# Optimization experiments

Hardware: AMD Instinct MI355X
Metric: run time of the kernel (lower is better)

Reference implementation:

```python
import jax, jax.numpy as jnp
import numpy as np

N, K, B, D, T = 30000, 32, 8, 256, 10
NC = T + 1            # int_small_classes
LB_COL, UB_COL = 21, 22
INF = 1e18


def _ln(x, g, b, eps=1e-5):
    m = jnp.mean(x, axis=-1, keepdims=True)
    v = jnp.mean((x - m) ** 2, axis=-1, keepdims=True)
    return (x - m) * jax.lax.rsqrt(v + eps) * g + b


def _head(x, ng, nb, W1, b1, W2, b2, Wh, bh):
    # LayerNorm -> Linear -> GELU -> Linear -> GELU -> residual -> head (dropout off: eval)
    h = _ln(x, ng, nb)
    h = jax.nn.gelu(h @ W1.T + b1, approximate=False)
    h = jax.nn.gelu(h @ W2.T + b2, approximate=False)
    return (x + h) @ Wh.T + bh


def setup_inputs():
    key = jax.random.key(0)
    ks = jax.random.split(key, 32)
    s = 0.05
    inp = {}
    inp['evolved_tokens'] = jax.random.normal(ks[0], (B * K, D), jnp.float32)
    inp['var_batch'] = jnp.sort(jax.random.randint(ks[1], (N,), 0, B))
    aw = jax.random.uniform(ks[2], (N, K), jnp.float32)
    inp['attn_weights'] = aw / aw.sum(-1, keepdims=True)
    inp['var_types'] = jax.random.randint(ks[3], (N,), 0, 3)
    inp['z_var_0'] = jax.random.normal(ks[4], (N, D), jnp.float32)
    vf = 0.1 * jax.random.normal(ks[5], (N, 23), jnp.float32)
    lb = jnp.floor(jax.random.uniform(ks[6], (N,), minval=-5.0, maxval=0.0))
    ub = lb + jnp.floor(jax.random.uniform(ks[7], (N,), minval=0.0, maxval=30.0))
    ub = jnp.where(jax.random.uniform(ks[8], (N,)) < 0.1, 1e19, ub)
    inp['variable_features'] = vf.at[:, LB_COL].set(lb).at[:, UB_COL].set(ub)
    # deslice proj + fusion norm
    inp['Wp'] = s * jax.random.normal(ks[9], (D, D), jnp.float32)
    inp['bp'] = jnp.zeros((D,), jnp.float32)
    inp['fn_g'] = jnp.ones((D,), jnp.float32)
    inp['fn_b'] = jnp.zeros((D,), jnp.float32)
    # three decoder heads
    i = 10
    for name, out in (('bin', 1), ('ints', NC), ('intl', 1)):
        inp[name + '_ng'] = jnp.ones((D,), jnp.float32)
        inp[name + '_nb'] = jnp.zeros((D,), jnp.float32)
        inp[name + '_W1'] = s * jax.random.normal(ks[i], (D, D), jnp.float32)
        inp[name + '_b1'] = jnp.zeros((D,), jnp.float32)
        inp[name + '_W2'] = s * jax.random.normal(ks[i + 1], (D, D), jnp.float32)
        inp[name + '_b2'] = jnp.zeros((D,), jnp.float32)
        inp[name + '_Wh'] = s * jax.random.normal(ks[i + 2], (out, D), jnp.float32)
        inp[name + '_bh'] = (jnp.full((out,), -0.5, jnp.float32) if name == 'bin'
                             else jnp.zeros((out,), jnp.float32))
        i += 3
    return inp


def reference(evolved_tokens, var_batch, attn_weights, var_types, z_var_0,
              variable_features, Wp, bp, fn_g, fn_b,
              bin_ng, bin_nb, bin_W1, bin_b1, bin_W2, bin_b2, bin_Wh, bin_bh,
              ints_ng, ints_nb, ints_W1, ints_b1, ints_W2, ints_b2, ints_Wh, ints_bh,
              intl_ng, intl_nb, intl_W1, intl_b1, intl_W2, intl_b2, intl_Wh, intl_bh):
    # 1. deslice: attn_weights @ projected evolved tokens of the variable's graph
    proj = evolved_tokens @ Wp.T + bp          # [B*K, D]
    tok3 = proj.reshape(B, K, D)
    z_des = jnp.einsum('nk,nkd->nd', attn_weights, tok3[var_batch])  # [N, D]
    # 2. residual fusion + LayerNorm
    z_out = _ln(z_des + z_var_0, fn_g, fn_b)
    # 3. routing (extract_int_routing)
    lb = variable_features[:, LB_COL]
    ub = variable_features[:, UB_COL]
    is_int = var_types == 2
    finite = (jnp.abs(lb) < INF) & (jnp.abs(ub) < INF)
    mask_int_small = is_int & finite & ((ub - lb) <= T)
    mask_int_large = is_int & ~mask_int_small
    mask_bin = var_types == 1
    offsets = jnp.floor(lb)                                   # [N]
    ranges = jnp.clip(jnp.ceil(ub) - offsets + 1.0, 1.0, NC).astype(jnp.int32)  # [N]
    # 4. decode. Heads are evaluated densely on all N rows; the original's
    #    gather->MLP->scatter equals row-selection of these dense outputs.
    prob_bin = jax.nn.sigmoid(_head(z_out, bin_ng, bin_nb, bin_W1, bin_b1,
                                    bin_W2, bin_b2, bin_Wh, bin_bh))   # [N, 1]
    logits = _head(z_out, ints_ng, ints_nb, ints_W1, ints_b1,
                   ints_W2, ints_b2, ints_Wh, ints_bh)                 # [N, NC]
    valid = jnp.arange(NC)[None, :] < ranges[:, None]
    logits = jnp.where(valid, logits, -1e9)  # dynamic logit masking of invalid classes
    pred_large = _head(z_out, intl_ng, intl_nb, intl_W1, intl_b1,
                       intl_W2, intl_b2, intl_Wh, intl_bh)             # [N, 1]
    return (z_out, prob_bin, logits, pred_large,
            mask_bin, mask_int_small, mask_int_large, offsets, ranges)
```

## Files before the change

kernel.cpp:

```cpp
#include <hip/hip_runtime.h>
#include <math.h>

#define NV   30000
#define DD   256
#define KK   32
#define NCLS 11
#define NT   469

#define OZ  0
#define OPB 7680000
#define OLG 7710000
#define OPL 8040000
#define OMB 8070000
#define OMS 8100000
#define OML 8130000
#define OOF 8160000
#define ORG 8190000

typedef __bf16 bf16x8 __attribute__((ext_vector_type(8)));
typedef float  f32x4  __attribute__((ext_vector_type(4)));

__device__ __forceinline__ unsigned short f2b(float f) {
    unsigned u = __float_as_uint(f);
    u += 0x7fffu + ((u >> 16) & 1u);
    return (unsigned short)(u >> 16);
}

__device__ __forceinline__ float gelu_f(float x) {
    float x2 = x * x;
    float m = x * __builtin_fmaf(-0.0713548163f, x2, -1.5957691216f);
    float e = __expf(m);
    return x * __builtin_amdgcn_rcpf(1.0f + e);
}

__device__ __forceinline__ int swz(int row) { return (row + (row >> 3)) & 7; }
__device__ __forceinline__ int lidx(int row, int col) {
    return row * 256 + ((((col) >> 3) ^ swz(row)) << 3) + (col & 7);
}

struct WP {
    const float *W1, *ng, *nb, *b1, *W2, *Wh;
    unsigned short *W1e, *W2b, *Whb;
    float *b1e, *swh;
    int nc;
};

__global__ void k_prep(const float* __restrict__ et, const float* __restrict__ Wp,
                       const float* __restrict__ bp, unsigned short* __restrict__ projb,
                       const float* __restrict__ vf, const int* __restrict__ vt,
                       float* __restrict__ out,
                       WP wa, WP wb, WP wc) {
    __shared__ float es[DD];
    __shared__ float red[4], red2[4];
    if (blockIdx.y == 0) {
        int r = blockIdx.x, c = threadIdx.x;
        es[c] = et[r * DD + c];
        __syncthreads();
        const float4* w4 = (const float4*)(Wp + c * DD);
        float acc = bp[c];
#pragma unroll 16
        for (int d = 0; d < DD / 4; ++d) {
            float4 w = w4[d];
            acc += es[4 * d] * w.x + es[4 * d + 1] * w.y + es[4 * d + 2] * w.z + es[4 * d + 3] * w.w;
        }
        projb[r * DD + c] = f2b(acc);
        return;
    }
    if (blockIdx.y == 4) {
        int n = blockIdx.x * 256 + threadIdx.x;
        if (n < NV) {
            float lb = vf[n * 23 + 21], ub = vf[n * 23 + 22];
            int t = vt[n];
            bool is_int = (t == 2);
            bool finite = (fabsf(lb) < 1e18f) && (fabsf(ub) < 1e18f);
            bool small_ = is_int && finite && (ub - lb <= 10.0f);
            float off = floorf(lb);
            float rngf = ceilf(ub) - off + 1.0f;
            rngf = fminf(fmaxf(rngf, 1.0f), (float)NCLS);
            out[OMB + n] = (t == 1) ? 1.0f : 0.0f;
            out[OMS + n] = small_ ? 1.0f : 0.0f;
            out[OML + n] = (is_int && !small_) ? 1.0f : 0.0f;
            out[OOF + n] = off;
            out[ORG + n] = (float)((int)rngf);
        }
        return;
    }
    WP wp = (blockIdx.y == 1) ? wa : ((blockIdx.y == 2) ? wb : wc);
    int j = blockIdx.x, d = threadIdx.x;
    float v1 = wp.W1[j * DD + d];
    wp.W1e[j * DD + d] = f2b(v1 * wp.ng[d]);
    wp.W2b[j * DD + d] = f2b(wp.W2[j * DD + d]);
    float p2 = 0.f;
    if (j < 16) {
        p2 = (j < wp.nc) ? wp.Wh[j * DD + d] : 0.f;
        wp.Whb[j * DD + d] = f2b(p2);
    }
    float p = v1 * wp.nb[d];
#pragma unroll
    for (int m = 1; m < 64; m <<= 1) { p += __shfl_xor(p, m); p2 += __shfl_xor(p2, m); }
    if ((d & 63) == 0) { red[d >> 6] = p; red2[d >> 6] = p2; }
    __syncthreads();
    if (d == 0) {
        wp.b1e[j] = wp.b1[j] + red[0] + red[1] + red[2] + red[3];
        if (j < 16) wp.swh[j] = red2[0] + red2[1] + red2[2] + red2[3];
    }
}

__global__ __launch_bounds__(256)
void k_zout(const unsigned short* __restrict__ projb, const int* __restrict__ vb,
            const float* __restrict__ aw, const float* __restrict__ z0,
            const float* __restrict__ g, const float* __restrict__ b,
            float* __restrict__ out, unsigned short* __restrict__ zhat,
            float2* __restrict__ zstat) {
    int wv = threadIdx.x >> 6, lane = threadIdx.x & 63;
    int n0r = blockIdx.x * 8 + wv * 2;
    if (n0r >= NV) return;
    bool ok1 = (n0r + 1) < NV;
    int b0 = vb[n0r];
    int b1i = ok1 ? vb[n0r + 1] : b0;
    float aw0 = aw[(size_t)n0r * KK + (lane & 31)];
    float aw1 = ok1 ? aw[(size_t)(n0r + 1) * KK + (lane & 31)] : 0.f;
    const ushort4* pr0 = (const ushort4*)(projb + (size_t)b0 * KK * DD);
    const ushort4* pr1 = (const ushort4*)(projb + (size_t)b1i * KK * DD);
    float4 acc0 = ((const float4*)(z0 + (size_t)n0r * DD))[lane];
    float4 acc1 = ok1 ? ((const float4*)(z0 + (size_t)(n0r + 1) * DD))[lane]
                      : make_float4(0.f, 0.f, 0.f, 0.f);
#pragma unroll 4
    for (int k = 0; k < KK; ++k) {
        float a0 = __shfl(aw0, k), a1 = __shfl(aw1, k);
        ushort4 p0 = pr0[k * 64 + lane];
        ushort4 p1 = pr1[k * 64 + lane];
        acc0.x += a0 * __uint_as_float((unsigned)p0.x << 16);
        acc0.y += a0 * __uint_as_float((unsigned)p0.y << 16);
        acc0.z += a0 * __uint_as_float((unsigned)p0.z << 16);
        acc0.w += a0 * __uint_as_float((unsigned)p0.w << 16);
        acc1.x += a1 * __uint_as_float((unsigned)p1.x << 16);
        acc1.y += a1 * __uint_as_float((unsigned)p1.y << 16);
        acc1.z += a1 * __uint_as_float((unsigned)p1.z << 16);
        acc1.w += a1 * __uint_as_float((unsigned)p1.w << 16);
    }
    float s0 = acc0.x + acc0.y + acc0.z + acc0.w;
    float q0 = acc0.x * acc0.x + acc0.y * acc0.y + acc0.z * acc0.z + acc0.w * acc0.w;
    float s1 = acc1.x + acc1.y + acc1.z + acc1.w;
    float q1 = acc1.x * acc1.x + acc1.y * acc1.y + acc1.z * acc1.z + acc1.w * acc1.w;
#pragma unroll
    for (int m = 1; m < 64; m <<= 1) {
        s0 += __shfl_xor(s0, m); q0 += __shfl_xor(q0, m);
        s1 += __shfl_xor(s1, m); q1 += __shfl_xor(q1, m);
    }
    float4 g4 = ((const float4*)g)[lane], b4 = ((const float4*)b)[lane];
#pragma unroll
    for (int rr = 0; rr < 2; ++rr) {
        int n = n0r + rr;
        if (rr && !ok1) break;
        float4 acc = rr ? acc1 : acc0;
        float s = rr ? s1 : s0, q = rr ? q1 : q0;
        float mean = s * (1.f / DD);
        float var  = q * (1.f / DD) - mean * mean;
        float rs   = rsqrtf(var + 1e-5f);
        float4 z;
        z.x = (acc.x - mean) * rs * g4.x + b4.x;
        z.y = (acc.y - mean) * rs * g4.y + b4.y;
        z.z = (acc.z - mean) * rs * g4.z + b4.z;
        z.w = (acc.w - mean) * rs * g4.w + b4.w;
        ((float4*)(out + OZ + (size_t)n * DD))[lane] = z;
        float s2 = z.x + z.y + z.z + z.w;
        float q2 = z.x * z.x + z.y * z.y + z.z * z.z + z.w * z.w;
#pragma unroll
        for (int m = 1; m < 64; m <<= 1) { s2 += __shfl_xor(s2, m); q2 += __shfl_xor(q2, m); }
        float m2 = s2 * (1.f / DD);
        float v2 = q2 * (1.f / DD) - m2 * m2;
        float r2 = rsqrtf(v2 + 1e-5f);
        ushort4 zh;
        zh.x = f2b((z.x - m2) * r2); zh.y = f2b((z.y - m2) * r2);
        zh.z = f2b((z.z - m2) * r2); zh.w = f2b((z.w - m2) * r2);
        int rl = n & 63;
        int c = lane >> 1;
        int pc = (c & ~7) | ((c & 7) ^ swz(rl));
        *(ushort4*)(zhat + (size_t)(n & ~63) * 256 + rl * 256 + pc * 8 + (lane & 1) * 4) = zh;
        if (lane == 0) zstat[n] = make_float2((v2 + 1e-5f) * r2, m2);
    }
}

struct HeadP {
    const unsigned short *W1e, *W2b, *Whb;
    const float *b1e, *b2, *bh, *swh;
    int nc;
};

__global__ __launch_bounds__(512, 4)
void k_heads(const unsigned short* __restrict__ zhat, const float2* __restrict__ zstat,
             const float* __restrict__ ranges,
             HeadP h0, HeadP h1p, HeadP h2p,
             float* __restrict__ opb, float* __restrict__ olg, float* __restrict__ opl) {
    __shared__ unsigned short hl[64 * 256];
    __shared__ float b1s[DD], b2s[DD];
    __shared__ float rs2s[64], m2s[64];
    __shared__ float swhs[16], bhs[16];

    int head = blockIdx.x / NT;
    int tile = blockIdx.x % NT;
    HeadP hp = (head == 0) ? h0 : ((head == 1) ? h1p : h2p);
    int nc = hp.nc;
    int n0 = tile * 64;
    int tid = threadIdx.x;

    {
        const uint4* src = (const uint4*)(zhat + (size_t)n0 * 256);
        uint4* dst = (uint4*)hl;
#pragma unroll
        for (int j = 0; j < 4; ++j) dst[tid + j * 512] = src[tid + j * 512];
    }
    if (tid < 256) b1s[tid] = hp.b1e[tid];
    else           b2s[tid - 256] = hp.b2[tid - 256];
    if (tid < 64) {
        int n = n0 + tid;
        float2 st = (n < NV) ? zstat[n] : make_float2(0.f, 0.f);
        rs2s[tid] = st.x; m2s[tid] = st.y;
    } else if (tid < 80) {
        swhs[tid - 64] = hp.swh[tid - 64];
    } else if (tid < 96) {
        int o = tid - 80;
        bhs[o] = (o < nc) ? hp.bh[o] : 0.f;
    }

    int lane = tid & 63, wv = tid >> 6;
    int l15 = lane & 15, lq = lane >> 4;
    int nb0 = wv * 32;

    f32x4 acc[4][2];
#pragma unroll
    for (int mt = 0; mt < 4; ++mt)
#pragma unroll
        for (int nt = 0; nt < 2; ++nt) acc[mt][nt] = f32x4{0.f, 0.f, 0.f, 0.f};

    __syncthreads();

    {
        const unsigned short* Bb = hp.W1e + (size_t)(nb0 + l15) * DD + lq * 8;
        bf16x8 b[2][2], a[4];
#pragma unroll
        for (int nt = 0; nt < 2; ++nt) b[0][nt] = *(const bf16x8*)(Bb + nt * 16 * DD);
#pragma unroll
        for (int ks = 0; ks < 8; ++ks) {
            int cur = ks & 1;
            if (ks < 7) {
#pragma unroll
                for (int nt = 0; nt < 2; ++nt)
                    b[cur ^ 1][nt] = *(const bf16x8*)(Bb + nt * 16 * DD + (ks + 1) * 32);
            }
            int ck = ks * 4 + lq;
#pragma unroll
            for (int mt = 0; mt < 4; ++mt) {
                int row = mt * 16 + l15;
                int ph = (ck & ~7) | ((ck & 7) ^ swz(row));
                a[mt] = *(const bf16x8*)(hl + row * 256 + ph * 8);
            }
#pragma unroll
            for (int nt = 0; nt < 2; ++nt)
#pragma unroll
                for (int mt = 0; mt < 4; ++mt)
                    acc[mt][nt] = __builtin_amdgcn_mfma_f32_16x16x32_bf16(a[mt], b[cur][nt], acc[mt][nt], 0, 0, 0);
        }
    }
    __syncthreads();

#pragma unroll
    for (int nt = 0; nt < 2; ++nt) {
        int col = nb0 + nt * 16 + l15;
        float bias = b1s[col];
#pragma unroll
        for (int mt = 0; mt < 4; ++mt)
#pragma unroll
            for (int r = 0; r < 4; ++r) {
                int row = mt * 16 + lq * 4 + r;
                hl[lidx(row, col)] = f2b(gelu_f(acc[mt][nt][r] + bias));
            }
    }
    __syncthreads();

#pragma unroll
    for (int mt = 0; mt < 4; ++mt)
#pragma unroll
        for (int nt = 0; nt < 2; ++nt) acc[mt][nt] = f32x4{0.f, 0.f, 0.f, 0.f};
    {
        const unsigned short* Bb = hp.W2b + (size_t)(nb0 + l15) * DD + lq * 8;
        bf16x8 b[2][2], a[4];
#pragma unroll
        for (int nt = 0; nt < 2; ++nt) b[0][nt] = *(const bf16x8*)(Bb + nt * 16 * DD);
#pragma unroll
        for (int ks = 0; ks < 8; ++ks) {
            int cur = ks & 1;
            if (ks < 7) {
#pragma unroll
                for (int nt = 0; nt < 2; ++nt)
                    b[cur ^ 1][nt] = *(const bf16x8*)(Bb + nt * 16 * DD + (ks + 1) * 32);
            }
            int ck = ks * 4 + lq;
#pragma unroll
            for (int mt = 0; mt < 4; ++mt) {
                int row = mt * 16 + l15;
                int ph = (ck & ~7) | ((ck & 7) ^ swz(row));
                a[mt] = *(const bf16x8*)(hl + row * 256 + ph * 8);
            }
#pragma unroll
            for (int nt = 0; nt < 2; ++nt)
#pragma unroll
                for (int mt = 0; mt < 4; ++mt)
                    acc[mt][nt] = __builtin_amdgcn_mfma_f32_16x16x32_bf16(a[mt], b[cur][nt], acc[mt][nt], 0, 0, 0);
        }
    }

#pragma unroll
    for (int nt = 0; nt < 2; ++nt) {
        float bias = b2s[nb0 + nt * 16 + l15];
#pragma unroll
        for (int mt = 0; mt < 4; ++mt)
#pragma unroll
            for (int r = 0; r < 4; ++r)
                acc[mt][nt][r] = gelu_f(acc[mt][nt][r] + bias);
    }
    __syncthreads();

#pragma unroll
    for (int nt = 0; nt < 2; ++nt) {
        int col = nb0 + nt * 16 + l15;
#pragma unroll
        for (int mt = 0; mt < 4; ++mt)
#pragma unroll
            for (int r = 0; r < 4; ++r) {
                int row = mt * 16 + lq * 4 + r;
                hl[lidx(row, col)] = f2b(acc[mt][nt][r]);
            }
    }

    f32x4 accP[4], accZ[4];
#pragma unroll
    for (int mt = 0; mt < 4; ++mt) { accP[mt] = f32x4{0.f, 0.f, 0.f, 0.f}; accZ[mt] = f32x4{0.f, 0.f, 0.f, 0.f}; }
    {
        const unsigned short* Wb = hp.Whb + (size_t)l15 * DD + nb0 + lq * 8;
        const unsigned short* zt = zhat + (size_t)n0 * 256;
        bf16x8 bP = *(const bf16x8*)(Wb);
        int ck = (nb0 >> 3) + lq;
#pragma unroll
        for (int mt = 0; mt < 4; ++mt) {
            int row = mt * 16 + l15;
            int ph = (ck & ~7) | ((ck & 7) ^ swz(row));
            bf16x8 aP = *(const bf16x8*)(hl + row * 256 + ph * 8);
            bf16x8 aZ = *(const bf16x8*)(zt + row * 256 + ph * 8);
            accP[mt] = __builtin_amdgcn_mfma_f32_16x16x32_bf16(aP, bP, accP[mt], 0, 0, 0);
            accZ[mt] = __builtin_amdgcn_mfma_f32_16x16x32_bf16(aZ, bP, accZ[mt], 0, 0, 0);
        }
    }
    __syncthreads();

#pragma unroll
    for (int mt = 0; mt < 4; ++mt) {
        int rb = mt * 16 + lq * 4;
#pragma unroll
        for (int r = 0; r < 4; ++r) {
            float pv = accP[mt][r] + rs2s[rb + r] * accZ[mt][r];
            float* pp = (float*)(hl + (rb + r) * 256 + nb0);
            pp[l15] = pv;
        }
    }
    __syncthreads();

    for (int idx = tid; idx < 64 * nc; idx += 512) {
        int row, o;
        if (nc == 1) { row = idx; o = 0; }
        else { row = idx / NCLS; o = idx - row * NCLS; }
        int n = n0 + row;
        if (n < NV) {
            float val = bhs[o] + m2s[row] * swhs[o];
#pragma unroll
            for (int w2 = 0; w2 < 8; ++w2)
                val += ((const float*)(hl + row * 256 + w2 * 32))[o];
            if (head == 0)      opb[n] = __builtin_amdgcn_rcpf(1.f + __expf(-val));
            else if (head == 2) opl[n] = val;
            else {
                int rng = (int)ranges[n];
                olg[n * NCLS + o] = (o < rng) ? val : -1e9f;
            }
        }
    }
}

extern "C" void kernel_launch(void* const* d_in, const int* in_sizes, int n_in,
                              void* d_out, int out_size, void* d_ws, size_t ws_size,
                              hipStream_t stream) {
    const float* et = (const float*)d_in[0];
    const int*   vb = (const int*)d_in[1];
    const float* aw = (const float*)d_in[2];
    const int*   vt = (const int*)d_in[3];
    const float* z0 = (const float*)d_in[4];
    const float* vf = (const float*)d_in[5];
    const float* Wp = (const float*)d_in[6];
    const float* bp = (const float*)d_in[7];
    const float* fg = (const float*)d_in[8];
    const float* fb = (const float*)d_in[9];
    float* out = (float*)d_out;

    char* ws = (char*)d_ws;
    unsigned short* projb = (unsigned short*)ws;
    float* b1e           = (float*)(ws + 131072);
    unsigned short* W1e  = (unsigned short*)(ws + 134144);
    unsigned short* W2b  = (unsigned short*)(ws + 527360);
    unsigned short* Whb  = (unsigned short*)(ws + 920576);
    float* swh           = (float*)(ws + 945152);
    float2* zstat        = (float2*)(ws + 945408);
    unsigned short* zhat = (unsigned short*)(ws + 1185536);

    WP wps[3];
    for (int h = 0; h < 3; ++h) {
        wps[h].W1 = (const float*)d_in[12 + 8 * h];
        wps[h].ng = (const float*)d_in[10 + 8 * h];
        wps[h].nb = (const float*)d_in[11 + 8 * h];
        wps[h].b1 = (const float*)d_in[13 + 8 * h];
        wps[h].W2 = (const float*)d_in[14 + 8 * h];
        wps[h].Wh = (const float*)d_in[16 + 8 * h];
        wps[h].W1e = W1e + h * 65536;
        wps[h].W2b = W2b + h * 65536;
        wps[h].Whb = Whb + h * 4096;
        wps[h].b1e = b1e + h * 256;
        wps[h].swh = swh + h * 16;
        wps[h].nc  = (h == 1) ? NCLS : 1;
    }
    k_prep<<<dim3(256, 5), 256, 0, stream>>>(et, Wp, bp, projb, vf, vt, out,
                                             wps[0], wps[1], wps[2]);

    k_zout<<<3750, 256, 0, stream>>>(projb, vb, aw, z0, fg, fb, out, zhat, zstat);

    HeadP hps[3];
    for (int h = 0; h < 3; ++h) {
        hps[h].W1e = W1e + h * 65536;
        hps[h].W2b = W2b + h * 65536;
        hps[h].Whb = Whb + h * 4096;
        hps[h].b1e = b1e + h * 256;
        hps[h].b2  = (const float*)d_in[15 + 8 * h];
        hps[h].bh  = (const float*)d_in[17 + 8 * h];
        hps[h].swh = swh + h * 16;
        hps[h].nc  = (h == 1) ? NCLS : 1;
    }
    k_heads<<<3 * NT, 512, 0, stream>>>(zhat, zstat, out + ORG,
                                        hps[0], hps[1], hps[2],
                                        out + OPB, out + OLG, out + OPL);
}
```

Measured before the change: 250.2 us.

## Compute z_out gather-sum as MFMA GEMM and precompute head residual projection

k_zout now builds a 64x256 bf16 attention matrix per tile (attention weights scattered to the batch's 32 columns) and multiplies it by a transposed projection with MFMA, replacing per-row scalar gathers of projected tokens. The same kernel also computes the residual term zhat·Wh for all three heads and stores it, so k_heads no longer re-reads zhat for that. k_heads swaps operand roles so weights are the A operand, uses two LDS buffers to cut a barrier, and reorganises the final reduction. The costs are a larger LDS footprint, a mostly-zero dense A matrix doing wasted MFMA work, and bf16 rounding of the attention weights.

```diff
diff --git a/kernel.cpp b/kernel.cpp
--- a/kernel.cpp
+++ b/kernel.cpp
@@ -37,6 +37,9 @@
 __device__ __forceinline__ int lidx(int row, int col) {
     return row * 256 + ((((col) >> 3) ^ swz(row)) << 3) + (col & 7);
 }
+__device__ __forceinline__ int physchunk(int ck, int row) {
+    return (ck & ~7) | ((ck & 7) ^ swz(row));
+}
 
 struct WP {
     const float *W1, *ng, *nb, *b1, *W2, *Wh;
@@ -46,7 +49,7 @@
 };
 
 __global__ void k_prep(const float* __restrict__ et, const float* __restrict__ Wp,
-                       const float* __restrict__ bp, unsigned short* __restrict__ projb,
+                       const float* __restrict__ bp, unsigned short* __restrict__ projT,
                        const float* __restrict__ vf, const int* __restrict__ vt,
                        float* __restrict__ out,
                        WP wa, WP wb, WP wc) {
@@ -63,7 +66,7 @@
             float4 w = w4[d];
             acc += es[4 * d] * w.x + es[4 * d + 1] * w.y + es[4 * d + 2] * w.z + es[4 * d + 3] * w.w;
         }
-        projb[r * DD + c] = f2b(acc);
+        projT[c * DD + r] = f2b(acc);
         return;
     }
     if (blockIdx.y == 4) {
@@ -106,281 +109,369 @@
     }
 }
 
-__global__ __launch_bounds__(256)
-void k_zout(const unsigned short* __restrict__ projb, const int* __restrict__ vb,
+__global__ __launch_bounds__(512)
+void k_zout(const unsigned short* __restrict__ projT, const int* __restrict__ vb,
             const float* __restrict__ aw, const float* __restrict__ z0,
             const float* __restrict__ g, const float* __restrict__ b,
+            const unsigned short* __restrict__ Whb, const float* __restrict__ swh,
             float* __restrict__ out, unsigned short* __restrict__ zhat,
-            float2* __restrict__ zstat) {
-    int wv = threadIdx.x >> 6, lane = threadIdx.x & 63;
-    int n0r = blockIdx.x * 8 + wv * 2;
-    if (n0r >= NV) return;
-    bool ok1 = (n0r + 1) < NV;
-    int b0 = vb[n0r];
-    int b1i = ok1 ? vb[n0r + 1] : b0;
-    float aw0 = aw[(size_t)n0r * KK + (lane & 31)];
-    float aw1 = ok1 ? aw[(size_t)(n0r + 1) * KK + (lane & 31)] : 0.f;
-    const ushort4* pr0 = (const ushort4*)(projb + (size_t)b0 * KK * DD);
-    const ushort4* pr1 = (const ushort4*)(projb + (size_t)b1i * KK * DD);
-    float4 acc0 = ((const float4*)(z0 + (size_t)n0r * DD))[lane];
-    float4 acc1 = ok1 ? ((const float4*)(z0 + (size_t)(n0r + 1) * DD))[lane]
-                      : make_float4(0.f, 0.f, 0.f, 0.f);
-#pragma unroll 4
-    for (int k = 0; k < KK; ++k) {
-        float a0 = __shfl(aw0, k), a1 = __shfl(aw1, k);
-        ushort4 p0 = pr0[k * 64 + lane];
-        ushort4 p1 = pr1[k * 64 + lane];
-        acc0.x += a0 * __uint_as_float((unsigned)p0.x << 16);
-        acc0.y += a0 * __uint_as_float((unsigned)p0.y << 16);
-        acc0.z += a0 * __uint_as_float((unsigned)p0.z << 16);
-        acc0.w += a0 * __uint_as_float((unsigned)p0.w << 16);
-        acc1.x += a1 * __uint_as_float((unsigned)p1.x << 16);
-        acc1.y += a1 * __uint_as_float((unsigned)p1.y << 16);
-        acc1.z += a1 * __uint_as_float((unsigned)p1.z << 16);
-        acc1.w += a1 * __uint_as_float((unsigned)p1.w << 16);
-    }
-    float s0 = acc0.x + acc0.y + acc0.z + acc0.w;
-    float q0 = acc0.x * acc0.x + acc0.y * acc0.y + acc0.z * acc0.z + acc0.w * acc0.w;
-    float s1 = acc1.x + acc1.y + acc1.z + acc1.w;
-    float q1 = acc1.x * acc1.x + acc1.y * acc1.y + acc1.z * acc1.z + acc1.w * acc1.w;
-#pragma unroll
-    for (int m = 1; m < 64; m <<= 1) {
-        s0 += __shfl_xor(s0, m); q0 += __shfl_xor(q0, m);
-        s1 += __shfl_xor(s1, m); q1 += __shfl_xor(q1, m);
-    }
-    float4 g4 = ((const float4*)g)[lane], b4 = ((const float4*)b)[lane];
-#pragma unroll
-    for (int rr = 0; rr < 2; ++rr) {
-        int n = n0r + rr;
-        if (rr && !ok1) break;
-        float4 acc = rr ? acc1 : acc0;
-        float s = rr ? s1 : s0, q = rr ? q1 : q0;
+            float* __restrict__ zwhT) {
+    __shared__ unsigned short Al[64 * 256];
+    __shared__ float sqs[64 * 8], sqq[64 * 8];
+    __shared__ float mvm[64], mvr[64], sig[64];
+    __shared__ float gs[DD], bs[DD];
+    __shared__ float swhs[48];
+    int tid = threadIdx.x;
+    int lane = tid & 63, wv = tid >> 6;
+    int l15 = lane & 15, lq = lane >> 4;
+    int n0 = blockIdx.x * 64;
+
+    if (tid < 256) gs[tid] = g[tid];
+    else           bs[tid - 256] = b[tid - 256];
+    if (tid < 48) swhs[tid] = swh[tid];
+    {
+        uint4 z4 = make_uint4(0, 0, 0, 0);
+        uint4* dst = (uint4*)Al;
+#pragma unroll
+        for (int j = 0; j < 4; ++j) dst[tid + j * 512] = z4;
+    }
+    __syncthreads();
+    {
+        int r = tid >> 3, sub = tid & 7;
+        int n = n0 + r;
+        if (n < NV) {
+            int bb = vb[n];
+            float4 a4 = *(const float4*)(aw + (size_t)n * KK + sub * 4);
+            int j0 = bb * 32 + sub * 4;
+            int phys = r * 256 + (physchunk(j0 >> 3, r) << 3) + (j0 & 7);
+            ushort4 u;
+            u.x = f2b(a4.x); u.y = f2b(a4.y); u.z = f2b(a4.z); u.w = f2b(a4.w);
+            *(ushort4*)(Al + phys) = u;
+        }
+    }
+    __syncthreads();
+
+    int nb0 = wv * 32;
+    f32x4 acc[4][2];
+#pragma unroll
+    for (int mt = 0; mt < 4; ++mt)
+#pragma unroll
+        for (int nt = 0; nt < 2; ++nt) acc[mt][nt] = f32x4{0.f, 0.f, 0.f, 0.f};
+
+    {
+        const unsigned short* Bb = projT + (size_t)(nb0 + l15) * DD + lq * 8;
+        bf16x8 bfr[2][2], afr[4];
+#pragma unroll
+        for (int nt = 0; nt < 2; ++nt) bfr[0][nt] = *(const bf16x8*)(Bb + nt * 16 * DD);
+#pragma unroll
+        for (int ks = 0; ks < 8; ++ks) {
+            int cur = ks & 1;
+            if (ks < 7) {
+#pragma unroll
+                for (int nt = 0; nt < 2; ++nt)
+                    bfr[cur ^ 1][nt] = *(const bf16x8*)(Bb + nt * 16 * DD + (ks + 1) * 32);
+            }
+            int ck = ks * 4 + lq;
+#pragma unroll
+            for (int mt = 0; mt < 4; ++mt) {
+                int row = mt * 16 + l15;
+                afr[mt] = *(const bf16x8*)(Al + row * 256 + (physchunk(ck, row) << 3));
+            }
+#pragma unroll
+            for (int nt = 0; nt < 2; ++nt)
+#pragma unroll
+                for (int mt = 0; mt < 4; ++mt)
+                    acc[mt][nt] = __builtin_amdgcn_mfma_f32_16x16x32_bf16(afr[mt], bfr[cur][nt], acc[mt][nt], 0, 0, 0);
+        }
+    }
+#pragma unroll
+    for (int mt = 0; mt < 4; ++mt)
+#pragma unroll
+        for (int nt = 0; nt < 2; ++nt) {
+            int col = nb0 + nt * 16 + l15;
+#pragma unroll
+            for (int r = 0; r < 4; ++r) {
+                int n = n0 + mt * 16 + lq * 4 + r;
+                float zv = (n < NV) ? z0[(size_t)n * DD + col] : 0.f;
+                acc[mt][nt][r] += zv;
+            }
+        }
+#pragma unroll
+    for (int mt = 0; mt < 4; ++mt)
+#pragma unroll
+        for (int r = 0; r < 4; ++r) {
+            float s = acc[mt][0][r] + acc[mt][1][r];
+            float q = acc[mt][0][r] * acc[mt][0][r] + acc[mt][1][r] * acc[mt][1][r];
+#pragma unroll
+            for (int m = 1; m < 16; m <<= 1) { s += __shfl_xor(s, m); q += __shfl_xor(q, m); }
+            if (l15 == 0) { int row = mt * 16 + lq * 4 + r; sqs[row * 8 + wv] = s; sqq[row * 8 + wv] = q; }
+        }
+    __syncthreads();
+    if (tid < 64) {
+        float s = 0.f, q = 0.f;
+#pragma unroll
+        for (int w = 0; w < 8; ++w) { s += sqs[tid * 8 + w]; q += sqq[tid * 8 + w]; }
         float mean = s * (1.f / DD);
         float var  = q * (1.f / DD) - mean * mean;
-        float rs   = rsqrtf(var + 1e-5f);
-        float4 z;
-        z.x = (acc.x - mean) * rs * g4.x + b4.x;
-        z.y = (acc.y - mean) * rs * g4.y + b4.y;
-        z.z = (acc.z - mean) * rs * g4.z + b4.z;
-        z.w = (acc.w - mean) * rs * g4.w + b4.w;
-        ((float4*)(out + OZ + (size_t)n * DD))[lane] = z;
-        float s2 = z.x + z.y + z.z + z.w;
-        float q2 = z.x * z.x + z.y * z.y + z.z * z.z + z.w * z.w;
-#pragma unroll
-        for (int m = 1; m < 64; m <<= 1) { s2 += __shfl_xor(s2, m); q2 += __shfl_xor(q2, m); }
-        float m2 = s2 * (1.f / DD);
-        float v2 = q2 * (1.f / DD) - m2 * m2;
+        mvm[tid] = mean; mvr[tid] = rsqrtf(var + 1e-5f);
+    }
+    __syncthreads();
+    float zb[4][2][4];
+#pragma unroll
+    for (int mt = 0; mt < 4; ++mt)
+#pragma unroll
+        for (int nt = 0; nt < 2; ++nt) {
+            int col = nb0 + nt * 16 + l15;
+#pragma unroll
+            for (int r = 0; r < 4; ++r) {
+                int row = mt * 16 + lq * 4 + r;
+                float z = (acc[mt][nt][r] - mvm[row]) * mvr[row] * gs[col] + bs[col];
+                zb[mt][nt][r] = z;
+                int n = n0 + row;
+                if (n < NV) out[OZ + (size_t)n * DD + col] = z;
+            }
+        }
+#pragma unroll
+    for (int mt = 0; mt < 4; ++mt)
+#pragma unroll
+        for (int r = 0; r < 4; ++r) {
+            float s = zb[mt][0][r] + zb[mt][1][r];
+            float q = zb[mt][0][r] * zb[mt][0][r] + zb[mt][1][r] * zb[mt][1][r];
+#pragma unroll
+            for (int m = 1; m < 16; m <<= 1) { s += __shfl_xor(s, m); q += __shfl_xor(q, m); }
+            if (l15 == 0) { int row = mt * 16 + lq * 4 + r; sqs[row * 8 + wv] = s; sqq[row * 8 + wv] = q; }
+        }
+    __syncthreads();
+    if (tid < 64) {
+        float s = 0.f, q = 0.f;
+#pragma unroll
+        for (int w = 0; w < 8; ++w) { s += sqs[tid * 8 + w]; q += sqq[tid * 8 + w]; }
+        float m2 = s * (1.f / DD);
+        float v2 = q * (1.f / DD) - m2 * m2;
         float r2 = rsqrtf(v2 + 1e-5f);
-        ushort4 zh;
-        zh.x = f2b((z.x - m2) * r2); zh.y = f2b((z.y - m2) * r2);
-        zh.z = f2b((z.z - m2) * r2); zh.w = f2b((z.w - m2) * r2);
-        int rl = n & 63;
-        int c = lane >> 1;
-        int pc = (c & ~7) | ((c & 7) ^ swz(rl));
-        *(ushort4*)(zhat + (size_t)(n & ~63) * 256 + rl * 256 + pc * 8 + (lane & 1) * 4) = zh;
-        if (lane == 0) zstat[n] = make_float2((v2 + 1e-5f) * r2, m2);
+        mvm[tid] = m2; mvr[tid] = r2; sig[tid] = (v2 + 1e-5f) * r2;
+    }
+    __syncthreads();
+#pragma unroll
+    for (int mt = 0; mt < 4; ++mt)
+#pragma unroll
+        for (int nt = 0; nt < 2; ++nt) {
+            int col = nb0 + nt * 16 + l15;
+#pragma unroll
+            for (int r = 0; r < 4; ++r) {
+                int row = mt * 16 + lq * 4 + r;
+                Al[lidx(row, col)] = f2b((zb[mt][nt][r] - mvm[row]) * mvr[row]);
+            }
+        }
+    __syncthreads();
+    if (wv < 4) {
+        f32x4 ac2[3];
+#pragma unroll
+        for (int mf = 0; mf < 3; ++mf) ac2[mf] = f32x4{0.f, 0.f, 0.f, 0.f};
+        const unsigned short* Ab = Whb + (size_t)l15 * DD + lq * 8;
+        int rowb = wv * 16 + l15;
+#pragma unroll
+        for (int ks = 0; ks < 8; ++ks) {
+            int ck = ks * 4 + lq;
+            bf16x8 bb2 = *(const bf16x8*)(Al + rowb * 256 + (physchunk(ck, rowb) << 3));
+#pragma unroll
+            for (int mf = 0; mf < 3; ++mf) {
+                bf16x8 aa2 = *(const bf16x8*)(Ab + (size_t)mf * 16 * DD + ks * 32);
+                ac2[mf] = __builtin_amdgcn_mfma_f32_16x16x32_bf16(aa2, bb2, ac2[mf], 0, 0, 0);
+            }
+        }
+        int nl = wv * 16 + l15;
+        float sg = sig[nl], mu = mvm[nl];
+#pragma unroll
+        for (int mf = 0; mf < 3; ++mf)
+#pragma unroll
+            for (int r = 0; r < 4; ++r) {
+                int o = mf * 16 + lq * 4 + r;
+                zwhT[(size_t)blockIdx.x * 3072 + o * 64 + nl] = sg * ac2[mf][r] + mu * swhs[o];
+            }
+    }
+    {
+        uint4* dstg = (uint4*)(zhat + (size_t)n0 * 256);
+        const uint4* srcl = (const uint4*)Al;
+#pragma unroll
+        for (int j = 0; j < 4; ++j) dstg[tid + j * 512] = srcl[tid + j * 512];
     }
 }
 
 struct HeadP {
     const unsigned short *W1e, *W2b, *Whb;
-    const float *b1e, *b2, *bh, *swh;
+    const float *b1e, *b2, *bh;
     int nc;
 };
 
 __global__ __launch_bounds__(512, 4)
-void k_heads(const unsigned short* __restrict__ zhat, const float2* __restrict__ zstat,
+void k_heads(const unsigned short* __restrict__ zhat, const float* __restrict__ zwhT,
              const float* __restrict__ ranges,
              HeadP h0, HeadP h1p, HeadP h2p,
              float* __restrict__ opb, float* __restrict__ olg, float* __restrict__ opl) {
-    __shared__ unsigned short hl[64 * 256];
+    __shared__ unsigned short hl1[64 * 256];
+    __shared__ unsigned short hl2[64 * 256];
     __shared__ float b1s[DD], b2s[DD];
-    __shared__ float rs2s[64], m2s[64];
-    __shared__ float swhs[16], bhs[16];
+    __shared__ float zws[16 * 64];
+    __shared__ float rgs[64];
+    __shared__ float bhs[16];
 
     int head = blockIdx.x / NT;
     int tile = blockIdx.x % NT;
     HeadP hp = (head == 0) ? h0 : ((head == 1) ? h1p : h2p);
     int nc = hp.nc;
     int n0 = tile * 64;
-    int tid = threadIdx.x;
+    int tid = threadIdx.x, lane = tid & 63, wv = tid >> 6;
+    int l15 = lane & 15, lq = lane >> 4;
+    int M0 = wv * 32;
 
     {
         const uint4* src = (const uint4*)(zhat + (size_t)n0 * 256);
-        uint4* dst = (uint4*)hl;
+        uint4* dst = (uint4*)hl1;
 #pragma unroll
         for (int j = 0; j < 4; ++j) dst[tid + j * 512] = src[tid + j * 512];
     }
     if (tid < 256) b1s[tid] = hp.b1e[tid];
     else           b2s[tid - 256] = hp.b2[tid - 256];
-    if (tid < 64) {
-        int n = n0 + tid;
-        float2 st = (n < NV) ? zstat[n] : make_float2(0.f, 0.f);
-        rs2s[tid] = st.x; m2s[tid] = st.y;
-    } else if (tid < 80) {
-        swhs[tid - 64] = hp.swh[tid - 64];
-    } else if (tid < 96) {
-        int o = tid - 80;
-        bhs[o] = (o < nc) ? hp.bh[o] : 0.f;
-    }
-
-    int lane = tid & 63, wv = tid >> 6;
-    int l15 = lane & 15, lq = lane >> 4;
-    int nb0 = wv * 32;
-
-    f32x4 acc[4][2];
-#pragma unroll
-    for (int mt = 0; mt < 4; ++mt)
-#pragma unroll
-        for (int nt = 0; nt < 2; ++nt) acc[mt][nt] = f32x4{0.f, 0.f, 0.f, 0.f};
-
-    __syncthreads();
-
-    {
-        const unsigned short* Bb = hp.W1e + (size_t)(nb0 + l15) * DD + lq * 8;
-        bf16x8 b[2][2], a[4];
-#pragma unroll
-        for (int nt = 0; nt < 2; ++nt) b[0][nt] = *(const bf16x8*)(Bb + nt * 16 * DD);
+    ((float2*)zws)[tid] = ((const float2*)(zwhT + (size_t)(tile * 3 + head) * 1024))[tid];
+    if (tid < 64) { int n = n0 + tid; rgs[tid] = (n < NV) ? ranges[n] : 0.f; }
+    else if (tid < 80) { int o = tid - 64; bhs[o] = (o < nc) ? hp.bh[o] : 0.f; }
+    __syncthreads();
+
+    f32x4 acc[2][4];
+#pragma unroll
+    for (int mt = 0; mt < 2; ++mt)
+#pragma unroll
+        for (int nt = 0; nt < 4; ++nt) acc[mt][nt] = f32x4{0.f, 0.f, 0.f, 0.f};
+
+    {
+        const unsigned short* Ab = hp.W1e + (size_t)(M0 + l15) * DD + lq * 8;
+        bf16x8 afr[2][2], bfr[4];
+#pragma unroll
+        for (int mt = 0; mt < 2; ++mt) afr[0][mt] = *(const bf16x8*)(Ab + mt * 16 * DD);
 #pragma unroll
         for (int ks = 0; ks < 8; ++ks) {
             int cur = ks & 1;
             if (ks < 7) {
 #pragma unroll
-                for (int nt = 0; nt < 2; ++nt)
-                    b[cur ^ 1][nt] = *(const bf16x8*)(Bb + nt * 16 * DD + (ks + 1) * 32);
+                for (int mt = 0; mt < 2; ++mt)
+                    afr[cur ^ 1][mt] = *(const bf16x8*)(Ab + mt * 16 * DD + (ks + 1) * 32);
             }
             int ck = ks * 4 + lq;
 #pragma unroll
-            for (int mt = 0; mt < 4; ++mt) {
-                int row = mt * 16 + l15;
-                int ph = (ck & ~7) | ((ck & 7) ^ swz(row));
-                a[mt] = *(const bf16x8*)(hl + row * 256 + ph * 8);
-            }
-#pragma unroll
-            for (int nt = 0; nt < 2; ++nt)
-#pragma unroll
-                for (int mt = 0; mt < 4; ++mt)
-                    acc[mt][nt] = __builtin_amdgcn_mfma_f32_16x16x32_bf16(a[mt], b[cur][nt], acc[mt][nt], 0, 0, 0);
-        }
-    }
-    __syncthreads();
-
-#pragma unroll
-    for (int nt = 0; nt < 2; ++nt) {
-        int col = nb0 + nt * 16 + l15;
-        float bias = b1s[col];
-#pragma unroll
-        for (int mt = 0; mt < 4; ++mt)
-#pragma unroll
-            for (int r = 0; r < 4; ++r) {
-                int row = mt * 16 + lq * 4 + r;
-                hl[lidx(row, col)] = f2b(gelu_f(acc[mt][nt][r] + bias));
-            }
-    }
-    __syncthreads();
-
-#pragma unroll
-    for (int mt = 0; mt < 4; ++mt)
-#pragma unroll
-        for (int nt = 0; nt < 2; ++nt) acc[mt][nt] = f32x4{0.f, 0.f, 0.f, 0.f};
-    {
-        const unsigned short* Bb = hp.W2b + (size_t)(nb0 + l15) * DD + lq * 8;
-        bf16x8 b[2][2], a[4];
-#pragma unroll
-        for (int nt = 0; nt < 2; ++nt) b[0][nt] = *(const bf16x8*)(Bb + nt * 16 * DD);
+            for (int nt = 0; nt < 4; ++nt) {
+                int row = nt * 16 + l15;
+                bfr[nt] = *(const bf16x8*)(hl1 + row * 256 + (physchunk(ck, row) << 3));
+            }
+#pragma unroll
+            for (int nt = 0; nt < 4; ++nt)
+#pragma unroll
+                for (int mt = 0; mt < 2; ++mt)
+                    acc[mt][nt] = __builtin_amdgcn_mfma_f32_16x16x32_bf16(afr[cur][mt], bfr[nt], acc[mt][nt], 0, 0, 0);
+        }
+    }
+#pragma unroll
+    for (int mt = 0; mt < 2; ++mt) {
+        int jb = M0 + mt * 16 + lq * 4;
+        float4 bias = *(const float4*)(b1s + jb);
+        int chunk = jb >> 3;
+#pragma unroll
+        for (int nt = 0; nt < 4; ++nt) {
+            int n = nt * 16 + l15;
+            ushort4 u;
+            u.x = f2b(gelu_f(acc[mt][nt][0] + bias.x));
+            u.y = f2b(gelu_f(acc[mt][nt][1] + bias.y));
+            u.z = f2b(gelu_f(acc[mt][nt][2] + bias.z));
+            u.w = f2b(gelu_f(acc[mt][nt][3] + bias.w));
+            *(ushort4*)(hl2 + n * 256 + (physchunk(chunk, n) << 3) + (jb & 7)) = u;
+        }
+    }
+    __syncthreads();
+
+#pragma unroll
+    for (int mt = 0; mt < 2; ++mt)
+#pragma unroll
+        for (int nt = 0; nt < 4; ++nt) acc[mt][nt] = f32x4{0.f, 0.f, 0.f, 0.f};
+    {
+        const unsigned short* Ab = hp.W2b + (size_t)(M0 + l15) * DD + lq * 8;
+        bf16x8 afr[2][2], bfr[4];
+#pragma unroll
+        for (int mt = 0; mt < 2; ++mt) afr[0][mt] = *(const bf16x8*)(Ab + mt * 16 * DD);
 #pragma unroll
         for (int ks = 0; ks < 8; ++ks) {
             int cur = ks & 1;
             if (ks < 7) {
 #pragma unroll
-                for (int nt = 0; nt < 2; ++nt)
-                    b[cur ^ 1][nt] = *(const bf16x8*)(Bb + nt * 16 * DD + (ks + 1) * 32);
+                for (int mt = 0; mt < 2; ++mt)
+                    afr[cur ^ 1][mt] = *(const bf16x8*)(Ab + mt * 16 * DD + (ks + 1) * 32);
             }
             int ck = ks * 4 + lq;
 #pragma unroll
-            for (int mt = 0; mt < 4; ++mt) {
-                int row = mt * 16 + l15;
-                int ph = (ck & ~7) | ((ck & 7) ^ swz(row));
-                a[mt] = *(const bf16x8*)(hl + row * 256 + ph * 8);
-            }
-#pragma unroll
-            for (int nt = 0; nt < 2; ++nt)
-#pragma unroll
-                for (int mt = 0; mt < 4; ++mt)
-                    acc[mt][nt] = __builtin_amdgcn_mfma_f32_16x16x32_bf16(a[mt], b[cur][nt], acc[mt][nt], 0, 0, 0);
-        }
-    }
-
-#pragma unroll
-    for (int nt = 0; nt < 2; ++nt) {
-        float bias = b2s[nb0 + nt * 16 + l15];
-#pragma unroll
-        for (int mt = 0; mt < 4; ++mt)
+            for (int nt = 0; nt < 4; ++nt) {
+                int row = nt * 16 + l15;
+                bfr[nt] = *(const bf16x8*)(hl2 + row * 256 + (physchunk(ck, row) << 3));
+            }
+#pragma unroll
+            for (int nt = 0; nt < 4; ++nt)
+#pragma unroll
+                for (int mt = 0; mt < 2; ++mt)
+                    acc[mt][nt] = __builtin_amdgcn_mfma_f32_16x16x32_bf16(afr[cur][mt], bfr[nt], acc[mt][nt], 0, 0, 0);
+        }
+    }
+#pragma unroll
+    for (int mt = 0; mt < 2; ++mt) {
+        int jb = M0 + mt * 16 + lq * 4;
+        float4 bias = *(const float4*)(b2s + jb);
+        int chunk = jb >> 3;
+#pragma unroll
+        for (int nt = 0; nt < 4; ++nt) {
+            int n = nt * 16 + l15;
+            ushort4 u;
+            u.x = f2b(gelu_f(acc[mt][nt][0] + bias.x));
+            u.y = f2b(gelu_f(acc[mt][nt][1] + bias.y));
+            u.z = f2b(gelu_f(acc[mt][nt][2] + bias.z));
+            u.w = f2b(gelu_f(acc[mt][nt][3] + bias.w));
+            *(ushort4*)(hl1 + n * 256 + (physchunk(chunk, n) << 3) + (jb & 7)) = u;
+        }
+    }
+    __syncthreads();
+
+    f32x4 ap[4];
+#pragma unroll
+    for (int nt = 0; nt < 4; ++nt) ap[nt] = f32x4{0.f, 0.f, 0.f, 0.f};
+    {
+        bf16x8 afr = *(const bf16x8*)(hp.Whb + (size_t)l15 * DD + wv * 32 + lq * 8);
+        int ck = wv * 4 + lq;
+#pragma unroll
+        for (int nt = 0; nt < 4; ++nt) {
+            int row = nt * 16 + l15;
+            bf16x8 bfr = *(const bf16x8*)(hl1 + row * 256 + (physchunk(ck, row) << 3));
+            ap[nt] = __builtin_amdgcn_mfma_f32_16x16x32_bf16(afr, bfr, ap[nt], 0, 0, 0);
+        }
+    }
+    {
+        float* pb = (float*)hl2;
+#pragma unroll
+        for (int nt = 0; nt < 4; ++nt)
 #pragma unroll
             for (int r = 0; r < 4; ++r)
-                acc[mt][nt][r] = gelu_f(acc[mt][nt][r] + bias);
-    }
-    __syncthreads();
-
-#pragma unroll
-    for (int nt = 0; nt < 2; ++nt) {
-        int col = nb0 + nt * 16 + l15;
-#pragma unroll
-        for (int mt = 0; mt < 4; ++mt)
-#pragma unroll
-            for (int r = 0; r < 4; ++r) {
-                int row = mt * 16 + lq * 4 + r;
-                hl[lidx(row, col)] = f2b(acc[mt][nt][r]);
-            }
-    }
-
-    f32x4 accP[4], accZ[4];
-#pragma unroll
-    for (int mt = 0; mt < 4; ++mt) { accP[mt] = f32x4{0.f, 0.f, 0.f, 0.f}; accZ[mt] = f32x4{0.f, 0.f, 0.f, 0.f}; }
-    {
-        const unsigned short* Wb = hp.Whb + (size_t)l15 * DD + nb0 + lq * 8;
-        const unsigned short* zt = zhat + (size_t)n0 * 256;
-        bf16x8 bP = *(const bf16x8*)(Wb);
-        int ck = (nb0 >> 3) + lq;
-#pragma unroll
-        for (int mt = 0; mt < 4; ++mt) {
-            int row = mt * 16 + l15;
-            int ph = (ck & ~7) | ((ck & 7) ^ swz(row));
-            bf16x8 aP = *(const bf16x8*)(hl + row * 256 + ph * 8);
-            bf16x8 aZ = *(const bf16x8*)(zt + row * 256 + ph * 8);
-            accP[mt] = __builtin_amdgcn_mfma_f32_16x16x32_bf16(aP, bP, accP[mt], 0, 0, 0);
-            accZ[mt] = __builtin_amdgcn_mfma_f32_16x16x32_bf16(aZ, bP, accZ[mt], 0, 0, 0);
-        }
-    }
-    __syncthreads();
-
-#pragma unroll
-    for (int mt = 0; mt < 4; ++mt) {
-        int rb = mt * 16 + lq * 4;
-#pragma unroll
-        for (int r = 0; r < 4; ++r) {
-            float pv = accP[mt][r] + rs2s[rb + r] * accZ[mt][r];
-            float* pp = (float*)(hl + (rb + r) * 256 + nb0);
-            pp[l15] = pv;
-        }
-    }
-    __syncthreads();
-
+                pb[wv * 1024 + (lq * 4 + r) * 64 + nt * 16 + l15] = ap[nt][r];
+    }
+    __syncthreads();
+
+    const float* pb = (const float*)hl2;
     for (int idx = tid; idx < 64 * nc; idx += 512) {
-        int row, o;
-        if (nc == 1) { row = idx; o = 0; }
-        else { row = idx / NCLS; o = idx - row * NCLS; }
-        int n = n0 + row;
-        if (n < NV) {
-            float val = bhs[o] + m2s[row] * swhs[o];
-#pragma unroll
-            for (int w2 = 0; w2 < 8; ++w2)
-                val += ((const float*)(hl + row * 256 + w2 * 32))[o];
-            if (head == 0)      opb[n] = __builtin_amdgcn_rcpf(1.f + __expf(-val));
-            else if (head == 2) opl[n] = val;
+        int o = idx >> 6, n = idx & 63;
+        float val = bhs[o] + zws[o * 64 + n];
+#pragma unroll
+        for (int w = 0; w < 8; ++w) val += pb[w * 1024 + o * 64 + n];
+        int ng = n0 + n;
+        if (ng < NV) {
+            if (head == 0)      opb[ng] = __builtin_amdgcn_rcpf(1.f + __expf(-val));
+            else if (head == 2) opl[ng] = val;
             else {
-                int rng = (int)ranges[n];
-                olg[n * NCLS + o] = (o < rng) ? val : -1e9f;
+                int rng = (int)rgs[n];
+                olg[(size_t)ng * NCLS + o] = (o < rng) ? val : -1e9f;
             }
         }
     }
@@ -402,14 +493,14 @@
     float* out = (float*)d_out;
 
     char* ws = (char*)d_ws;
-    unsigned short* projb = (unsigned short*)ws;
+    unsigned short* projT = (unsigned short*)ws;
     float* b1e           = (float*)(ws + 131072);
     unsigned short* W1e  = (unsigned short*)(ws + 134144);
     unsigned short* W2b  = (unsigned short*)(ws + 527360);
     unsigned short* Whb  = (unsigned short*)(ws + 920576);
     float* swh           = (float*)(ws + 945152);
-    float2* zstat        = (float2*)(ws + 945408);
-    unsigned short* zhat = (unsigned short*)(ws + 1185536);
+    float* zwhT          = (float*)(ws + 945408);
+    unsigned short* zhat = (unsigned short*)(ws + 6708480);
 
     WP wps[3];
     for (int h = 0; h < 3; ++h) {
@@ -426,10 +517,11 @@
         wps[h].swh = swh + h * 16;
         wps[h].nc  = (h == 1) ? NCLS : 1;
     }
-    k_prep<<<dim3(256, 5), 256, 0, stream>>>(et, Wp, bp, projb, vf, vt, out,
+    k_prep<<<dim3(256, 5), 256, 0, stream>>>(et, Wp, bp, projT, vf, vt, out,
                                              wps[0], wps[1], wps[2]);
 
-    k_zout<<<3750, 256, 0, stream>>>(projb, vb, aw, z0, fg, fb, out, zhat, zstat);
+    k_zout<<<NT, 512, 0, stream>>>(projT, vb, aw, z0, fg, fb, Whb, swh,
+                                   out, zhat, zwhT);
 
     HeadP hps[3];
     for (int h = 0; h < 3; ++h) {
@@ -439,10 +531,9 @@
         hps[h].b1e = b1e + h * 256;
         hps[h].b2  = (const float*)d_in[15 + 8 * h];
         hps[h].bh  = (const float*)d_in[17 + 8 * h];
-        hps[h].swh = swh + h * 16;
         hps[h].nc  = (h == 1) ? NCLS : 1;
     }
-    k_heads<<<3 * NT, 512, 0, stream>>>(zhat, zstat, out + ORG,
+    k_heads<<<3 * NT, 512, 0, stream>>>(zhat, zwhT, out + ORG,
                                         hps[0], hps[1], hps[2],
                                         out + OPB, out + OLG, out + OPL);
 }
```

Result: faster. 244.8 us (-2.2%).
